# Optimization experiments

Measured on AMD Instinct MI355X. Metric: run time of the kernel, lower is better.

Reference implementation:

```python
import jax, jax.numpy as jnp
import numpy as np

B, T, N = 2048, 500, 64
DT = 0.25  # integration step
V_TH = 30.0

# Izhikevich behaviour params: (a, b, c, d, v0); u0 = b * v0
LLBN_P = (0.02, 0.20, -65.0, 6.0, -70.0)   # LLBN_behaviour (tonic-spiking-like)
EBN_P  = (0.02, 0.25, -55.0, 0.05, -64.0)  # phasic bursting
IFN_P  = (0.02, 0.25, -65.0, 6.0, -64.0)   # phasic spiking
TN_P   = (0.02, 0.20, -50.0, 2.0, -70.0)   # tonic bursting
MN_P   = IFN_P                              # phasic spiking


def izh_step(v, u, I, p):
    """One Euler step of the Izhikevich neuron; returns (spike, v_new, u_new)."""
    a, b, c, d, _ = p
    v_ = v + DT * (0.04 * v * v + 5.0 * v + 140.0 - u + I)
    u_ = u + DT * a * (b * v - u)
    z = (v_ >= V_TH).astype(v.dtype)
    v_new = jnp.where(z > 0, c, v_)
    u_new = u_ + z * d
    return z, v_new, u_new


def init_state(p, batch):
    a, b, c, d, v0 = p
    return jnp.full((batch,), v0, jnp.float32), jnp.full((batch,), b * v0, jnp.float32)


def setup_inputs() -> dict:
    key = jax.random.key(0)
    k1, k2 = jax.random.split(key)
    input_mat = jax.random.uniform(k1, (B, T, N), dtype=jnp.float32)
    weights_matrix = jax.random.uniform(k2, (24,), dtype=jnp.float32)
    return {"input_mat": input_mat, "weights_matrix": weights_matrix}


def _run(input_mat, w):
    # summed retinal drive per timestep; [B, T] -> [T, B] for scan
    zp1 = (input_mat * w[0]).sum(-1).T
    zp2 = (input_mat * w[12]).sum(-1).T

    vL, uL = init_state(LLBN_P, B); zL = jnp.zeros((B,), jnp.float32)
    vE, uE = init_state(EBN_P, B)
    vI, uI = init_state(IFN_P, B)
    vT, uT = init_state(TN_P, B); zT = jnp.zeros((B,), jnp.float32)
    vM, uM = init_state(MN_P, B)
    # channel 2 uses the SAME cells (self.LLBN/EBN/... are reused in the
    # original forward, so weights w[2],w[3],w[9],w[10] apply) with its own state
    vL2, uL2 = vL, uL; zL2 = zL
    vE2, uE2 = vE, uE
    vI2, uI2 = vI, uI
    vT2, uT2 = vT, uT; zT2 = zT
    vM2, uM2 = vM, uM

    carry0 = (vL, uL, zL, vE, uE, vI, uI, vT, uT, zT, vM, uM,
              vL2, uL2, zL2, vE2, uE2, vI2, uI2, vT2, uT2, zT2, vM2, uM2)

    def step(carry, zin):
        (vL, uL, zL, vE, uE, vI, uI, vT, uT, zT, vM, uM,
         vL2, uL2, zL2, vE2, uE2, vI2, uI2, vT2, uT2, zT2, vM2, uM2) = carry
        zp, zp2 = zin
        # --- channel 1 ---  (temp feedback is always 0 in the original: local var)
        z2, vL, uL = izh_step(vL, uL, w[2] * (zp * w[1]) + w[3] * zL, LLBN_P)
        z3, vE, uE = izh_step(vE, uE, zp * w[4] + z2 * w[5], EBN_P)
        z4, vI, uI = izh_step(vI, uI, z3 * w[6], IFN_P)
        z5, vT, uT = izh_step(vT, uT, w[9] * (z3 * w[8]) + w[10] * zT, TN_P)
        z6, vM, uM = izh_step(vM, uM, z5 * w[11], MN_P)
        # --- channel 2 ---
        z22, vL2, uL2 = izh_step(vL2, uL2, w[2] * (zp2 * w[13]) + w[3] * zL2, LLBN_P)
        z32, vE2, uE2 = izh_step(vE2, uE2, zp2 * w[16] + z22 * w[17], EBN_P)
        z42, vI2, uI2 = izh_step(vI2, uI2, z32 * w[18], IFN_P)
        z52, vT2, uT2 = izh_step(vT2, uT2, w[9] * (z32 * w[20]) + w[10] * zT2, TN_P)
        z62, vM2, uM2 = izh_step(vM2, uM2, z52 * w[23], MN_P)
        new_carry = (vL, uL, z2, vE, uE, vI, uI, vT, uT, z5, vM, uM,
                     vL2, uL2, z22, vE2, uE2, vI2, uI2, vT2, uT2, z52, vM2, uM2)
        outs = (z6, vM, z62, vM2,
                jnp.stack([z2, z3, z4, z5], -1),   # o_spikes_o [B,4]
                jnp.stack([vL, vE, vI, vT], -1))   # v_o        [B,4]
        return new_carry, outs

    _, (o_spikes, v, o_spikes2, v2, o_spikes_o, v_o) = jax.lax.scan(step, carry0, (zp1, zp2))
    # scan stacks on leading T axis -> move to [B, T, ...]
    tr = lambda a: jnp.moveaxis(a, 0, 1)
    return tr(o_spikes), tr(v), tr(o_spikes2), tr(v2), tr(o_spikes_o), tr(v_o)


def reference(input_mat, weights_matrix):
    return _run(input_mat, weights_matrix)
```

## Files before the change

### kernel.cpp

```cpp
#include <hip/hip_runtime.h>

#define B_ 2048
#define T_ 500
#define BT (B_ * T_)

__device__ __forceinline__ float izh_m(float& v, float& u, float I,
                                       float b, float c, float d, bool valid) {
    float t  = 0.04f * v * v + 5.0f * v + 140.0f - u + I;
    float v_ = v + 0.25f * t;
    float u_ = u + 0.005f * (b * v - u);
    float z  = (v_ >= 30.0f) ? 1.0f : 0.0f;
    float vn = (v_ >= 30.0f) ? c : v_;
    float un = u_ + z * d;
    if (!valid) { z = 0.f; vn = v; un = u; }
    v = vn; u = un;
    return z;
}

__device__ __forceinline__ float dpp_shr1(float x) {
    return __int_as_float(__builtin_amdgcn_update_dpp(
        0, __float_as_int(x), 0x111, 0xf, 0xf, true));
}

#define BAR() do {                                                             \
    asm volatile("s_waitcnt lgkmcnt(0)" ::: "memory");                         \
    __builtin_amdgcn_s_barrier();                                              \
    __builtin_amdgcn_sched_barrier(0);                                         \
} while (0)

__global__ __launch_bounds__(128) void fused_scan6_kernel(
        const float* __restrict__ in, const float* __restrict__ w24,
        float* __restrict__ out) {
    __shared__ float S_lds[128];
    __shared__ float ring[64 * 56];

    const int tid   = threadIdx.x;
    const int wid   = tid >> 6;
    const int lane  = tid & 63;
    const int bbase = blockIdx.x << 2;

    const int c     = lane >> 4;
    const int slot  = lane & 15;
    const int chl   = slot >> 3;
    const int role8 = slot & 7;

    const float a0   = chl ? w24[12] : w24[0];
    const float W1v  = chl ? w24[13] : w24[1];
    const float W4v  = chl ? w24[16] : w24[4];
    const float W5x  = chl ? w24[17] : w24[5];
    const float W6v  = chl ? w24[18] : w24[6];
    const float W8v  = chl ? w24[20] : w24[8];
    const float W11v = chl ? w24[23] : w24[11];
    const float W2 = w24[2], W3 = w24[3], W9 = w24[9], W10 = w24[10];

    float pb, pcc, pd, v, u, wA, wB, wC, wD;
    float fL = 0.f, fE = 0.f, fITM = 0.f;
    int offs;
    if (role8 == 0 || role8 == 4) {
        pb=0.20f; pcc=-65.f; pd=6.f;   v=-70.f; u=-14.f;
        wA=W2;  wB=W1v;  wC=0.f; wD=W3;  offs=0; fL=1.f;
    } else if (role8 == 1 || role8 == 5) {
        pb=0.25f; pcc=-55.f; pd=0.05f; v=-64.f; u=-16.f;
        wA=1.f; wB=W4v;  wC=W5x; wD=0.f; offs=3; fE=1.f;
    } else if (role8 == 2) {
        pb=0.25f; pcc=-65.f; pd=6.f;   v=-64.f; u=-16.f;
        wA=1.f; wB=W6v;  wC=0.f; wD=0.f; offs=6; fITM=1.f;
    } else if (role8 == 6) {
        pb=0.20f; pcc=-50.f; pd=2.f;   v=-70.f; u=-14.f;
        wA=W9;  wB=W8v;  wC=0.f; wD=W10; offs=6; fITM=1.f;
    } else if (role8 == 7) {
        pb=0.25f; pcc=-65.f; pd=6.f;   v=-64.f; u=-16.f;
        wA=1.f; wB=W11v; wC=0.f; wD=0.f; offs=9; fITM=1.f;
    } else {
        pb=0.25f; pcc=-65.f; pd=6.f;   v=-64.f; u=-16.f;
        wA=0.f; wB=0.f;  wC=0.f; wD=0.f; offs=9;
    }
    const bool wr = (chl == 0 && (role8 <= 2 || role8 == 6 || role8 == 7))
                 || (chl == 1 && role8 == 7);
    int p = 0;
    if (role8 == 1) p = 1;
    else if (role8 == 2) p = 2;
    else if (role8 == 6) p = 3;
    else if (role8 == 7) p = chl ? 5 : 4;
    const int ringoff = c * 14 + 2 * p;

    float z_last = 0.f, in_p1 = 0.f, in_p2 = 0.f;
    float zp1 = 0.f, zp2 = 0.f, zp3 = 0.f;

    const float* inb = in + (size_t)bbase * T_ * 64;
    float4 Ae[8], Ao[8], Be[8], Bo[8];

#define ISSUE(KK, BE, BO) {                                                    \
    const int t0i = 16 * (KK);                                                 \
    _Pragma("unroll")                                                          \
    for (int pp = 0; pp < 8; ++pp) {                                           \
        const int rt = pp * 8 + (lane >> 3);                                   \
        const int row = rt >> 4, tt = rt & 15;                                 \
        const int tcl = (t0i + tt <= 499) ? tt : 0;                            \
        const float* ap = inb + ((size_t)row * T_ + t0i + tcl) * 64            \
                              + (lane & 7) * 8;                                \
        BE[pp] = *(const float4*)ap;                                           \
        BO[pp] = *(const float4*)(ap + 4);                                     \
    }                                                                          \
}

#define REDUCE(KK, BE, BO) {                                                   \
    float* sw = S_lds + ((KK) & 1) * 64;                                       \
    const int t0r = 16 * (KK);                                                 \
    _Pragma("unroll")                                                          \
    for (int pp = 0; pp < 8; ++pp) {                                           \
        float4 e = BE[pp], o = BO[pp];                                         \
        float s = ((e.x + e.y) + (e.z + e.w)) + ((o.x + o.y) + (o.z + o.w));   \
        s += __shfl_xor(s, 1);                                                 \
        s += __shfl_xor(s, 2);                                                 \
        s += __shfl_xor(s, 4);                                                 \
        const int rt = pp * 8 + (lane >> 3);                                   \
        const int row = rt >> 4, tt = rt & 15;                                 \
        if ((lane & 7) == 0) sw[row * 16 + tt] = (t0r + tt <= 499) ? s : 0.f;  \
    }                                                                          \
}

#define SYS_ITER(SV, VEXPR, I_) {                                              \
    float in0 = in_p2;                                                         \
    in_p2 = in_p1;                                                             \
    in_p1 = dpp_shr1(z_last);                                                  \
    float zpc = (SV) * a0;                                                     \
    float X = (fL * zpc + fE * zp3) + fITM * in0;                              \
    float Isyn = wA * (X * wB) + wC * in0 + wD * z_last;                       \
    float znew = izh_m(v, u, Isyn, pb, pcc, pd, (VEXPR));                      \
    if (wr) *(float2*)(ringp + (I_) * 56) = make_float2(znew, v);              \
    zp3 = zp2; zp2 = zp1; zp1 = zpc;                                           \
    z_last = znew;                                                             \
}

#define GROUP16(VF)                                                            \
    SYS_ITER(g0.x, VF(0),  0)  SYS_ITER(g0.y, VF(1),  1)                       \
    SYS_ITER(g0.z, VF(2),  2)  SYS_ITER(g0.w, VF(3),  3)                       \
    SYS_ITER(g1.x, VF(4),  4)  SYS_ITER(g1.y, VF(5),  5)                       \
    SYS_ITER(g1.z, VF(6),  6)  SYS_ITER(g1.w, VF(7),  7)                       \
    SYS_ITER(g2.x, VF(8),  8)  SYS_ITER(g2.y, VF(9),  9)                       \
    SYS_ITER(g2.z, VF(10), 10) SYS_ITER(g2.w, VF(11), 11)                      \
    SYS_ITER(g3.x, VF(12), 12) SYS_ITER(g3.y, VF(13), 13)                      \
    SYS_ITER(g3.z, VF(14), 14) SYS_ITER(g3.w, VF(15), 15)

#define VF_PRO(i)  ((i) >= offs)
#define VF_ONE(i)  true
#define VF_EPI(i)  ((i) <= 3 + offs)

#define DUMP(K) {                                                              \
    const int td = lane & 15;                                                  \
    const int cc = lane >> 4;                                                  \
    const int t  = 16 * (K) - 9 + td;                                          \
    if (0 <= t && t <= 499) {                                                  \
        const float* rb = ring + cc * 14;                                      \
        float2 a2 = *(const float2*)&rb[((t)     & 63) * 56 + 0];              \
        float2 b2 = *(const float2*)&rb[((t + 3) & 63) * 56 + 2];              \
        float2 c1 = *(const float2*)&rb[((t + 6) & 63) * 56 + 4];              \
        float2 c2 = *(const float2*)&rb[((t + 6) & 63) * 56 + 6];              \
        float2 e1 = *(const float2*)&rb[((t + 9) & 63) * 56 + 8];              \
        float2 e2 = *(const float2*)&rb[((t + 9) & 63) * 56 + 10];             \
        const size_t g = (size_t)(bbase + cc) * T_ + t;                        \
        out[g]          = e1.x;                           \
        out[BT + g]     = e1.y;                           \
        out[2 * BT + g] = e2.x;                           \
        out[3 * BT + g] = e2.y;                           \
        ((float4*)out)[BT + g]     = make_float4(a2.x, b2.x, c1.x, c2.x);      \
        ((float4*)out)[2 * BT + g] = make_float4(a2.y, b2.y, c1.y, c2.y);      \
    }                                                                          \
}

#define SCANP(K, VFSEL) {                                                      \
    const float4* sp = (const float4*)(S_lds + ((K) & 1) * 64 + c * 16);       \
    float4 g0 = sp[0], g1 = sp[1], g2 = sp[2], g3 = sp[3];                     \
    float* ringp = ring + ((K) & 3) * 896 + ringoff;                           \
    __builtin_amdgcn_s_setprio(1);                                             \
    GROUP16(VFSEL)                                                             \
    __builtin_amdgcn_s_setprio(0);                                             \
}

    if (wid == 1) {
        ISSUE(0, Ae, Ao)
        REDUCE(0, Ae, Ao)
        ISSUE(1, Be, Bo)
    }
    BAR();

    for (int k = 0; k < 32; k += 2) {
        if (wid == 0) {
            if (k == 0) { SCANP(k, VF_PRO) } else { SCANP(k, VF_ONE) }
        } else {
            if (k + 2 < 32) { ISSUE(k + 2, Ae, Ao) }
            if (k + 1 < 32) { REDUCE(k + 1, Be, Bo) }
            if (k >= 1) { DUMP(k - 1) }
        }
        BAR();
        if (wid == 0) {
            if (k + 1 == 31) { SCANP(k + 1, VF_EPI) } else { SCANP(k + 1, VF_ONE) }
        } else {
            if (k + 3 < 32) { ISSUE(k + 3, Be, Bo) }
            if (k + 2 < 32) { REDUCE(k + 2, Ae, Ao) }
            DUMP(k)
        }
        BAR();
    }
    if (wid == 1) { DUMP(31) }

#undef ISSUE
#undef REDUCE
#undef SYS_ITER
#undef GROUP16
#undef VF_PRO
#undef VF_ONE
#undef VF_EPI
#undef DUMP
#undef SCANP
}

extern "C" void kernel_launch(void* const* d_in, const int* in_sizes, int n_in,
                              void* d_out, int out_size, void* d_ws, size_t ws_size,
                              hipStream_t stream) {
    const float* in = (const float*)d_in[0];
    const float* w  = (const float*)d_in[1];
    float* out = (float*)d_out;

    fused_scan6_kernel<<<512, 128, 0, stream>>>(in, w, out);
}
```

Measured before the change: 72.54 us.

## Replace producer/consumer two-wave blocks with single-wave per-batch scan kernel

The kernel changes from 128-thread blocks, where one wave loads and reduces inputs for 4 batch rows while another runs the scan, to one 64-lane wave per batch row that loads, reduces via shuffles and readlane, scans and dumps on its own. This removes LDS staging of the reduced drive and the block barriers, and launches 2048 blocks instead of 512 to spread the serial work over more waves. In exchange only 16 lanes do useful scan work and the other 48 are idle, and the load latency is no longer hidden by a separate producer wave.

```diff
diff --git a/kernel.cpp b/kernel.cpp
--- a/kernel.cpp
+++ b/kernel.cpp
@@ -22,24 +22,18 @@
         0, __float_as_int(x), 0x111, 0xf, 0xf, true));
 }
 
-#define BAR() do {                                                             \
-    asm volatile("s_waitcnt lgkmcnt(0)" ::: "memory");                         \
-    __builtin_amdgcn_s_barrier();                                              \
-    __builtin_amdgcn_sched_barrier(0);                                         \
-} while (0)
-
-__global__ __launch_bounds__(128) void fused_scan6_kernel(
+__device__ __forceinline__ float rlane(float x, int l) {
+    return __int_as_float(__builtin_amdgcn_readlane(__float_as_int(x), l));
+}
+
+__global__ __launch_bounds__(64, 2) void mono_scan_kernel(
         const float* __restrict__ in, const float* __restrict__ w24,
         float* __restrict__ out) {
-    __shared__ float S_lds[128];
-    __shared__ float ring[64 * 56];
-
-    const int tid   = threadIdx.x;
-    const int wid   = tid >> 6;
-    const int lane  = tid & 63;
-    const int bbase = blockIdx.x << 2;
-
-    const int c     = lane >> 4;
+    __shared__ float ring[32 * 14];
+
+    const int lane  = threadIdx.x;
+    const int b     = blockIdx.x;
+    const int grp   = lane >> 4;
     const int slot  = lane & 15;
     const int chl   = slot >> 3;
     const int role8 = slot & 7;
@@ -56,7 +50,10 @@
     float pb, pcc, pd, v, u, wA, wB, wC, wD;
     float fL = 0.f, fE = 0.f, fITM = 0.f;
     int offs;
-    if (role8 == 0 || role8 == 4) {
+    if (grp != 0) {
+        pb=0.25f; pcc=-65.f; pd=6.f;   v=-64.f; u=-16.f;
+        wA=0.f; wB=0.f;  wC=0.f; wD=0.f; offs=9;
+    } else if (role8 == 0 || role8 == 4) {
         pb=0.20f; pcc=-65.f; pd=6.f;   v=-70.f; u=-14.f;
         wA=W2;  wB=W1v;  wC=0.f; wD=W3;  offs=0; fL=1.f;
     } else if (role8 == 1 || role8 == 5) {
@@ -75,49 +72,47 @@
         pb=0.25f; pcc=-65.f; pd=6.f;   v=-64.f; u=-16.f;
         wA=0.f; wB=0.f;  wC=0.f; wD=0.f; offs=9;
     }
-    const bool wr = (chl == 0 && (role8 <= 2 || role8 == 6 || role8 == 7))
-                 || (chl == 1 && role8 == 7);
+    const bool wr = (grp == 0) &&
+        ((chl == 0 && (role8 <= 2 || role8 == 6 || role8 == 7)) ||
+         (chl == 1 && role8 == 7));
     int p = 0;
     if (role8 == 1) p = 1;
     else if (role8 == 2) p = 2;
     else if (role8 == 6) p = 3;
     else if (role8 == 7) p = chl ? 5 : 4;
-    const int ringoff = c * 14 + 2 * p;
+    const int ringoff = 2 * p;
 
     float z_last = 0.f, in_p1 = 0.f, in_p2 = 0.f;
     float zp1 = 0.f, zp2 = 0.f, zp3 = 0.f;
 
-    const float* inb = in + (size_t)bbase * T_ * 64;
-    float4 Ae[8], Ao[8], Be[8], Bo[8];
-
-#define ISSUE(KK, BE, BO) {                                                    \
-    const int t0i = 16 * (KK);                                                 \
+    const float* inb = in + (size_t)b * T_ * 64;
+    float4 L0[4], L1[4];
+    float sE0, sE1, sE2, sE3, sO0, sO1, sO2, sO3;
+
+#define ISSUE(M, BUF) {                                                        \
+    const int t0i = 16 * (M);                                                  \
     _Pragma("unroll")                                                          \
-    for (int pp = 0; pp < 8; ++pp) {                                           \
-        const int rt = pp * 8 + (lane >> 3);                                   \
-        const int row = rt >> 4, tt = rt & 15;                                 \
-        const int tcl = (t0i + tt <= 499) ? tt : 0;                            \
-        const float* ap = inb + ((size_t)row * T_ + t0i + tcl) * 64            \
-                              + (lane & 7) * 8;                                \
-        BE[pp] = *(const float4*)ap;                                           \
-        BO[pp] = *(const float4*)(ap + 4);                                     \
+    for (int q = 0; q < 4; ++q) {                                              \
+        const int tq = (t0i + 4 * q + 3 <= 499) ? 4 * q : 0;                   \
+        BUF[q] = *(const float4*)(inb + (size_t)(t0i + tq + grp) * 64          \
+                                      + slot * 4);                             \
     }                                                                          \
 }
 
-#define REDUCE(KK, BE, BO) {                                                   \
-    float* sw = S_lds + ((KK) & 1) * 64;                                       \
-    const int t0r = 16 * (KK);                                                 \
-    _Pragma("unroll")                                                          \
-    for (int pp = 0; pp < 8; ++pp) {                                           \
-        float4 e = BE[pp], o = BO[pp];                                         \
-        float s = ((e.x + e.y) + (e.z + e.w)) + ((o.x + o.y) + (o.z + o.w));   \
-        s += __shfl_xor(s, 1);                                                 \
-        s += __shfl_xor(s, 2);                                                 \
-        s += __shfl_xor(s, 4);                                                 \
-        const int rt = pp * 8 + (lane >> 3);                                   \
-        const int row = rt >> 4, tt = rt & 15;                                 \
-        if ((lane & 7) == 0) sw[row * 16 + tt] = (t0r + tt <= 499) ? s : 0.f;  \
-    }                                                                          \
+#define REDUCE(BUF, S0, S1, S2, S3) {                                          \
+    float s_; float4 vv_;                                                      \
+    vv_ = BUF[0]; s_ = (vv_.x + vv_.y) + (vv_.z + vv_.w);                      \
+    s_ += __shfl_xor(s_, 1); s_ += __shfl_xor(s_, 2);                          \
+    s_ += __shfl_xor(s_, 4); s_ += __shfl_xor(s_, 8); S0 = s_;                 \
+    vv_ = BUF[1]; s_ = (vv_.x + vv_.y) + (vv_.z + vv_.w);                      \
+    s_ += __shfl_xor(s_, 1); s_ += __shfl_xor(s_, 2);                          \
+    s_ += __shfl_xor(s_, 4); s_ += __shfl_xor(s_, 8); S1 = s_;                 \
+    vv_ = BUF[2]; s_ = (vv_.x + vv_.y) + (vv_.z + vv_.w);                      \
+    s_ += __shfl_xor(s_, 1); s_ += __shfl_xor(s_, 2);                          \
+    s_ += __shfl_xor(s_, 4); s_ += __shfl_xor(s_, 8); S2 = s_;                 \
+    vv_ = BUF[3]; s_ = (vv_.x + vv_.y) + (vv_.z + vv_.w);                      \
+    s_ += __shfl_xor(s_, 1); s_ += __shfl_xor(s_, 2);                          \
+    s_ += __shfl_xor(s_, 4); s_ += __shfl_xor(s_, 8); S3 = s_;                 \
 }
 
 #define SYS_ITER(SV, VEXPR, I_) {                                              \
@@ -128,38 +123,45 @@
     float X = (fL * zpc + fE * zp3) + fITM * in0;                              \
     float Isyn = wA * (X * wB) + wC * in0 + wD * z_last;                       \
     float znew = izh_m(v, u, Isyn, pb, pcc, pd, (VEXPR));                      \
-    if (wr) *(float2*)(ringp + (I_) * 56) = make_float2(znew, v);              \
+    if (wr) *(float2*)(ringp + (I_) * 14) = make_float2(znew, v);              \
     zp3 = zp2; zp2 = zp1; zp1 = zpc;                                           \
     z_last = znew;                                                             \
 }
 
-#define GROUP16(VF)                                                            \
-    SYS_ITER(g0.x, VF(0),  0)  SYS_ITER(g0.y, VF(1),  1)                       \
-    SYS_ITER(g0.z, VF(2),  2)  SYS_ITER(g0.w, VF(3),  3)                       \
-    SYS_ITER(g1.x, VF(4),  4)  SYS_ITER(g1.y, VF(5),  5)                       \
-    SYS_ITER(g1.z, VF(6),  6)  SYS_ITER(g1.w, VF(7),  7)                       \
-    SYS_ITER(g2.x, VF(8),  8)  SYS_ITER(g2.y, VF(9),  9)                       \
-    SYS_ITER(g2.z, VF(10), 10) SYS_ITER(g2.w, VF(11), 11)                      \
-    SYS_ITER(g3.x, VF(12), 12) SYS_ITER(g3.y, VF(13), 13)                      \
-    SYS_ITER(g3.z, VF(14), 14) SYS_ITER(g3.w, VF(15), 15)
+#define G16(S0, S1, S2, S3, VF)                                                \
+    SYS_ITER(rlane(S0,  0), VF(0),  0)  SYS_ITER(rlane(S0, 16), VF(1),  1)     \
+    SYS_ITER(rlane(S0, 32), VF(2),  2)  SYS_ITER(rlane(S0, 48), VF(3),  3)     \
+    SYS_ITER(rlane(S1,  0), VF(4),  4)  SYS_ITER(rlane(S1, 16), VF(5),  5)     \
+    SYS_ITER(rlane(S1, 32), VF(6),  6)  SYS_ITER(rlane(S1, 48), VF(7),  7)     \
+    SYS_ITER(rlane(S2,  0), VF(8),  8)  SYS_ITER(rlane(S2, 16), VF(9),  9)     \
+    SYS_ITER(rlane(S2, 32), VF(10), 10) SYS_ITER(rlane(S2, 48), VF(11), 11)    \
+    SYS_ITER(rlane(S3,  0), VF(12), 12) SYS_ITER(rlane(S3, 16), VF(13), 13)    \
+    SYS_ITER(rlane(S3, 32), VF(14), 14) SYS_ITER(rlane(S3, 48), VF(15), 15)
+
+#define G16_EPI(S0)                                                            \
+    SYS_ITER(rlane(S0,  0), VF_EPI(0),  0)  SYS_ITER(rlane(S0, 16), VF_EPI(1),  1) \
+    SYS_ITER(rlane(S0, 32), VF_EPI(2),  2)  SYS_ITER(rlane(S0, 48), VF_EPI(3),  3) \
+    SYS_ITER(0.f, VF_EPI(4),  4)  SYS_ITER(0.f, VF_EPI(5),  5)                 \
+    SYS_ITER(0.f, VF_EPI(6),  6)  SYS_ITER(0.f, VF_EPI(7),  7)                 \
+    SYS_ITER(0.f, VF_EPI(8),  8)  SYS_ITER(0.f, VF_EPI(9),  9)                 \
+    SYS_ITER(0.f, VF_EPI(10), 10) SYS_ITER(0.f, VF_EPI(11), 11)                \
+    SYS_ITER(0.f, VF_EPI(12), 12) SYS_ITER(0.f, VF_EPI(13), 13)                \
+    SYS_ITER(0.f, VF_EPI(14), 14) SYS_ITER(0.f, VF_EPI(15), 15)
 
 #define VF_PRO(i)  ((i) >= offs)
 #define VF_ONE(i)  true
 #define VF_EPI(i)  ((i) <= 3 + offs)
 
 #define DUMP(K) {                                                              \
-    const int td = lane & 15;                                                  \
-    const int cc = lane >> 4;                                                  \
-    const int t  = 16 * (K) - 9 + td;                                          \
-    if (0 <= t && t <= 499) {                                                  \
-        const float* rb = ring + cc * 14;                                      \
-        float2 a2 = *(const float2*)&rb[((t)     & 63) * 56 + 0];              \
-        float2 b2 = *(const float2*)&rb[((t + 3) & 63) * 56 + 2];              \
-        float2 c1 = *(const float2*)&rb[((t + 6) & 63) * 56 + 4];              \
-        float2 c2 = *(const float2*)&rb[((t + 6) & 63) * 56 + 6];              \
-        float2 e1 = *(const float2*)&rb[((t + 9) & 63) * 56 + 8];              \
-        float2 e2 = *(const float2*)&rb[((t + 9) & 63) * 56 + 10];             \
-        const size_t g = (size_t)(bbase + cc) * T_ + t;                        \
+    const int t = 16 * (K) - 9 + slot;                                         \
+    if (grp == 0 && 0 <= t && t <= 499) {                                      \
+        float2 a2 = *(const float2*)&ring[((t)     & 31) * 14 + 0];            \
+        float2 b2 = *(const float2*)&ring[((t + 3) & 31) * 14 + 2];            \
+        float2 c1 = *(const float2*)&ring[((t + 6) & 31) * 14 + 4];            \
+        float2 c2 = *(const float2*)&ring[((t + 6) & 31) * 14 + 6];            \
+        float2 e1 = *(const float2*)&ring[((t + 9) & 31) * 14 + 8];            \
+        float2 e2 = *(const float2*)&ring[((t + 9) & 31) * 14 + 10];           \
+        const size_t g = (size_t)b * T_ + t;                                   \
         out[g]          = e1.x;                           \
         out[BT + g]     = e1.y;                           \
         out[2 * BT + g] = e2.x;                           \
@@ -169,51 +171,38 @@
     }                                                                          \
 }
 
-#define SCANP(K, VFSEL) {                                                      \
-    const float4* sp = (const float4*)(S_lds + ((K) & 1) * 64 + c * 16);       \
-    float4 g0 = sp[0], g1 = sp[1], g2 = sp[2], g3 = sp[3];                     \
-    float* ringp = ring + ((K) & 3) * 896 + ringoff;                           \
-    __builtin_amdgcn_s_setprio(1);                                             \
-    GROUP16(VFSEL)                                                             \
-    __builtin_amdgcn_s_setprio(0);                                             \
-}
-
-    if (wid == 1) {
-        ISSUE(0, Ae, Ao)
-        REDUCE(0, Ae, Ao)
-        ISSUE(1, Be, Bo)
+    ISSUE(0, L0)
+    REDUCE(L0, sE0, sE1, sE2, sE3)
+    ISSUE(1, L1)
+
+    for (int k = 0; k < 32; k += 2) {
+        if (k + 2 < 32) { ISSUE(k + 2, L0) }
+        if (k + 1 < 32) { REDUCE(L1, sO0, sO1, sO2, sO3) }
+        {
+            float* ringp = ring + ringoff;
+            if (k == 0) { G16(sE0, sE1, sE2, sE3, VF_PRO) }
+            else        { G16(sE0, sE1, sE2, sE3, VF_ONE) }
+        }
+        DUMP(k)
+        if (k + 3 < 32) { ISSUE(k + 3, L1) }
+        if (k + 2 < 32) { REDUCE(L0, sE0, sE1, sE2, sE3) }
+        {
+            float* ringp = ring + 16 * 14 + ringoff;
+            if (k + 1 == 31) { G16_EPI(sO0) }
+            else             { G16(sO0, sO1, sO2, sO3, VF_ONE) }
+        }
+        DUMP(k + 1)
     }
-    BAR();
-
-    for (int k = 0; k < 32; k += 2) {
-        if (wid == 0) {
-            if (k == 0) { SCANP(k, VF_PRO) } else { SCANP(k, VF_ONE) }
-        } else {
-            if (k + 2 < 32) { ISSUE(k + 2, Ae, Ao) }
-            if (k + 1 < 32) { REDUCE(k + 1, Be, Bo) }
-            if (k >= 1) { DUMP(k - 1) }
-        }
-        BAR();
-        if (wid == 0) {
-            if (k + 1 == 31) { SCANP(k + 1, VF_EPI) } else { SCANP(k + 1, VF_ONE) }
-        } else {
-            if (k + 3 < 32) { ISSUE(k + 3, Be, Bo) }
-            if (k + 2 < 32) { REDUCE(k + 2, Ae, Ao) }
-            DUMP(k)
-        }
-        BAR();
-    }
-    if (wid == 1) { DUMP(31) }
 
 #undef ISSUE
 #undef REDUCE
 #undef SYS_ITER
-#undef GROUP16
+#undef G16
+#undef G16_EPI
 #undef VF_PRO
 #undef VF_ONE
 #undef VF_EPI
 #undef DUMP
-#undef SCANP
 }
 
 extern "C" void kernel_launch(void* const* d_in, const int* in_sizes, int n_in,
@@ -223,5 +212,5 @@
     const float* w  = (const float*)d_in[1];
     float* out = (float*)d_out;
 
-    fused_scan6_kernel<<<512, 128, 0, stream>>>(in, w, out);
-}
+    mono_scan_kernel<<<B_, 64, 0, stream>>>(in, w, out);
+}
```

Result: slower. 84.04 us (+15.8%).
